# Performance work log

Measured on AMD Instinct MI355X. Metric: run time of the kernel, lower is better.

## Reference

```python
import jax, jax.numpy as jnp
import numpy as np

N, D, M, H, FF, L = 8192, 14, 36, 256, 2048, 2  # rows, d_model, material feats, mlp hidden, ffn, layers
EPS = 1e-5


def _ln(x, g, b):
    mu = jnp.mean(x, axis=-1, keepdims=True)
    var = jnp.mean((x - mu) ** 2, axis=-1, keepdims=True)
    return (x - mu) * jax.lax.rsqrt(var + EPS) * g + b


def setup_inputs() -> dict:
    key = jax.random.key(0)
    ks = iter(jax.random.split(key, 32))
    p = lambda shape, fan: jax.random.normal(next(ks), shape, jnp.float32) * (fan ** -0.5)
    return {
        "x": jax.random.normal(next(ks), (N, D), jnp.float32),
        "y": jax.random.normal(next(ks), (N, M), jnp.float32),
        # 2 post-LN TransformerEncoderLayers (nhead=1, dim_feedforward=2048, relu)
        "attn_wqkv": p((L, 3 * D, D), D), "attn_bqkv": p((L, 3 * D), D),
        "attn_wo": p((L, D, D), D), "attn_bo": p((L, D), D),
        "ln1_g": jnp.ones((L, D)), "ln1_b": jnp.zeros((L, D)),
        "ff_w1": p((L, FF, D), D), "ff_b1": p((L, FF), D),
        "ff_w2": p((L, D, FF), FF), "ff_b2": p((L, D), FF),
        "ln2_g": jnp.ones((L, D)), "ln2_b": jnp.zeros((L, D)),
        "fc1_w": p((D, D), D), "fc1_b": p((D,), D),
        "fc2_w": p((1, D), D), "fc2_b": p((1,), D),
        "fc3_w": p((H, D + M + 1), D + M + 1), "fc3_b": p((H,), D + M + 1),
        "fc4_w": p((H, H), H), "fc4_b": p((H,), H),
        "fc5_w": p((1, H), H), "fc5_b": p((1,), H),
    }


def reference(x, y, attn_wqkv, attn_bqkv, attn_wo, attn_bo, ln1_g, ln1_b,
              ff_w1, ff_b1, ff_w2, ff_b2, ln2_g, ln2_b,
              fc1_w, fc1_b, fc2_w, fc2_b, fc3_w, fc3_b, fc4_w, fc4_b, fc5_w, fc5_b):
    h = x  # [N, D]; batch of size 1 squeezed away
    for l in range(L):
        qkv = h @ attn_wqkv[l].T + attn_bqkv[l]            # [N, 3D]
        q, k, v = jnp.split(qkv, 3, axis=-1)
        scores = (q @ k.T) * (D ** -0.5)                   # [N, N]
        a = jax.nn.softmax(scores, axis=-1) @ v            # [N, D]
        a = a @ attn_wo[l].T + attn_bo[l]
        h = _ln(h + a, ln1_g[l], ln1_b[l])
        f = jax.nn.relu(h @ ff_w1[l].T + ff_b1[l]) @ ff_w2[l].T + ff_b2[l]
        h = _ln(h + f, ln2_g[l], ln2_b[l])
    x1 = h @ fc1_w.T + fc1_b                               # [N, D]
    size_out = (x1 @ fc2_w.T + fc2_b)[:, 0]                # [N]

    # batched replacement of the per-row python loop
    size_int = size_out.astype(jnp.int32)                  # trunc toward zero, like .int()
    size_f = size_int.astype(jnp.float32)[:, None]         # [N, 1]
    reg_in = jnp.concatenate([size_f, x, y], axis=1)       # [N, 1+D+M]
    r = jax.nn.relu(reg_in @ fc3_w.T + fc3_b)
    r = jax.nn.relu(r @ fc4_w.T + fc4_b)
    reg_values = (r @ fc5_w.T + fc5_b)[:, 0]               # [N]
    reg_values = jnp.where(size_int != 0, reg_values, 0.0)
    return size_out, reg_values
```

## Files before the change

kernel.cpp:

```cpp
#include <hip/hip_runtime.h>
#include <math.h>

#define NN 8192
#define DD 14
#define DP 16
#define FF 2048
#define HID 256
#define LN_EPS 1e-5f
#define QSCALE (1.4426950408889634f / 3.7416573867739413f)

typedef short bf16x8 __attribute__((ext_vector_type(8)));
typedef float f32x4 __attribute__((ext_vector_type(4)));

#define LOAD16(dst, srcp) { \
  const float4* _p = (const float4*)(srcp); \
  float4 _a = _p[0], _b = _p[1], _c = _p[2], _d = _p[3]; \
  dst[0]=_a.x; dst[1]=_a.y; dst[2]=_a.z; dst[3]=_a.w; \
  dst[4]=_b.x; dst[5]=_b.y; dst[6]=_b.z; dst[7]=_b.w; \
  dst[8]=_c.x; dst[9]=_c.y; dst[10]=_c.z; dst[11]=_c.w; \
  dst[12]=_d.x; dst[13]=_d.y; dst[14]=_d.z; dst[15]=_d.w; }

#define STORE16(dstp, src) { \
  float4* _p = (float4*)(dstp); \
  _p[0] = make_float4(src[0], src[1], src[2], src[3]); \
  _p[1] = make_float4(src[4], src[5], src[6], src[7]); \
  _p[2] = make_float4(src[8], src[9], src[10], src[11]); \
  _p[3] = make_float4(src[12], src[13], src[14], src[15]); }

static __device__ __forceinline__ float fast_exp2(float x) {
#if __has_builtin(__builtin_amdgcn_exp2f)
  return __builtin_amdgcn_exp2f(x);
#else
  return exp2f(x);
#endif
}

static __device__ __forceinline__ unsigned short bf_hi(float x) {
  return (unsigned short)(__float_as_uint(x) >> 16);
}
static __device__ __forceinline__ float bf_hi_f(float x) {
  return __uint_as_float(__float_as_uint(x) & 0xffff0000u);
}

static __device__ __forceinline__ void split8(const float* pv, bf16x8* ph, bf16x8* pl) {
  #pragma unroll
  for (int i = 0; i < 8; i++) {
    unsigned int u = __float_as_uint(pv[i]);
    (*ph)[i] = (short)(u >> 16);
    float rr = pv[i] - __uint_as_float(u & 0xffff0000u);
    (*pl)[i] = (short)(__float_as_uint(rr) >> 16);
  }
}

static __device__ __forceinline__ void qkv_compute_store(
    int r, const float* hr, const float* __restrict__ wqkv,
    const float* __restrict__ bqkv, unsigned int* __restrict__ Qpack,
    unsigned int* __restrict__ KB1, unsigned int* __restrict__ KB2,
    unsigned short* __restrict__ VhiT, unsigned short* __restrict__ VloT) {
  float q[14], k[14], v[14];
  #pragma unroll 6
  for (int c = 0; c < 42; c++) {
    const float* w = wqkv + c * 14;
    float s = bqkv[c];
    #pragma unroll
    for (int d = 0; d < 14; d++) s = fmaf(hr[d], w[d], s);
    if (c < 14)       q[c] = s * QSCALE;
    else if (c < 28)  k[c - 14] = s;
    else              v[c - 28] = s;
  }
  unsigned int qp[16], k1[16], k2[16];
  unsigned short qh[14], ql[14], kh[14], kl[14];
  #pragma unroll
  for (int d = 0; d < 14; d++) {
    qh[d] = bf_hi(q[d]);
    ql[d] = bf_hi(q[d] - bf_hi_f(q[d]));
    kh[d] = bf_hi(k[d]);
    kl[d] = bf_hi(k[d] - bf_hi_f(k[d]));
  }
  #pragma unroll
  for (int i = 0; i < 7; i++) {
    qp[i]     = (unsigned int)qh[2*i] | ((unsigned int)qh[2*i+1] << 16);
    qp[8 + i] = (unsigned int)ql[2*i] | ((unsigned int)ql[2*i+1] << 16);
    k1[i]     = (unsigned int)kh[2*i] | ((unsigned int)kh[2*i+1] << 16);
    k1[8 + i] = k1[i];
    k2[i]     = (unsigned int)kl[2*i] | ((unsigned int)kl[2*i+1] << 16);
    k2[8 + i] = k2[i];
  }
  qp[7] = 0; qp[15] = 0; k1[7] = 0; k1[15] = 0; k2[7] = 0; k2[15] = 0;
  uint4* Qp4 = (uint4*)(Qpack + (size_t)r * 16);
  uint4* K14 = (uint4*)(KB1 + (size_t)r * 16);
  uint4* K24 = (uint4*)(KB2 + (size_t)r * 16);
  #pragma unroll
  for (int i = 0; i < 4; i++) {
    Qp4[i] = make_uint4(qp[4*i], qp[4*i+1], qp[4*i+2], qp[4*i+3]);
    K14[i] = make_uint4(k1[4*i], k1[4*i+1], k1[4*i+2], k1[4*i+3]);
    K24[i] = make_uint4(k2[4*i], k2[4*i+1], k2[4*i+2], k2[4*i+3]);
  }
  #pragma unroll
  for (int d = 0; d < 14; d++) {
    VhiT[(size_t)d * NN + r] = bf_hi(v[d]);
    VloT[(size_t)d * NN + r] = bf_hi(v[d] - bf_hi_f(v[d]));
  }
  VhiT[(size_t)14 * NN + r] = 0x3F80;
  VhiT[(size_t)15 * NN + r] = 0;
  VloT[(size_t)14 * NN + r] = 0;
  VloT[(size_t)15 * NN + r] = 0;
}

static __device__ __forceinline__ void store_apack(unsigned int* dst, const float* o) {
  unsigned int qp[16];
  unsigned short hh[14], ll[14];
  #pragma unroll
  for (int d = 0; d < 14; d++) {
    hh[d] = bf_hi(o[d]);
    ll[d] = bf_hi(o[d] - bf_hi_f(o[d]));
  }
  #pragma unroll
  for (int i = 0; i < 7; i++) {
    qp[i]     = (unsigned int)hh[2*i] | ((unsigned int)hh[2*i+1] << 16);
    qp[8 + i] = (unsigned int)ll[2*i] | ((unsigned int)ll[2*i+1] << 16);
  }
  qp[7] = 0; qp[15] = 0;
  uint4* d4 = (uint4*)dst;
  #pragma unroll
  for (int i = 0; i < 4; i++)
    d4[i] = make_uint4(qp[4*i], qp[4*i+1], qp[4*i+2], qp[4*i+3]);
}

static __device__ __forceinline__ void combine_ln1(
    const float* srow, const float* hr, const float* __restrict__ wo,
    const float* __restrict__ bo, const float* __restrict__ g,
    const float* __restrict__ b, float* o) {
  float L = srow[14];
  float inv = 1.f / L;
  float a[14];
  #pragma unroll
  for (int d = 0; d < 14; d++) a[d] = srow[d] * inv;
  float xx[14];
  #pragma unroll
  for (int i = 0; i < 14; i++) {
    float s = bo[i];
    #pragma unroll
    for (int d = 0; d < 14; d++) s = fmaf(wo[i * 14 + d], a[d], s);
    xx[i] = hr[i] + s;
  }
  float mu = 0.f;
  #pragma unroll
  for (int i = 0; i < 14; i++) mu += xx[i];
  mu *= (1.f / 14.f);
  float var = 0.f;
  #pragma unroll
  for (int i = 0; i < 14; i++) { float tt = xx[i] - mu; var = fmaf(tt, tt, var); }
  var *= (1.f / 14.f);
  float rs = rsqrtf(var + LN_EPS);
  #pragma unroll
  for (int i = 0; i < 14; i++) o[i] = fmaf((xx[i] - mu) * rs, g[i], b[i]);
  o[14] = 0.f; o[15] = 0.f;
}

__global__ void pack_all(const float* __restrict__ w3, const float* __restrict__ w4,
                         const float* __restrict__ ffw1, const float* __restrict__ ffw2,
                         const float* __restrict__ x, const float* __restrict__ wqkv,
                         const float* __restrict__ bqkv, float* __restrict__ h,
                         unsigned int* __restrict__ Qpack,
                         unsigned int* __restrict__ KB1, unsigned int* __restrict__ KB2,
                         unsigned short* __restrict__ VhiT, unsigned short* __restrict__ VloT,
                         unsigned short* __restrict__ B3h, unsigned short* __restrict__ B3l,
                         unsigned short* __restrict__ B4h, unsigned short* __restrict__ B4l,
                         unsigned int* __restrict__ W1B1, unsigned int* __restrict__ W1B2,
                         unsigned short* __restrict__ W2h, unsigned short* __restrict__ W2l) {
  const int blk = blockIdx.x, tid = threadIdx.x;
  if (blk < 32) {
    int t = blk * 256 + tid;
    int lane = t & 63, ks = (t >> 6) & 7, nt = t >> 9;
    int n = nt * 16 + (lane & 15);
    int k0 = ks * 32 + (lane >> 4) * 8;
    unsigned int h4[4], l4[4];
    #pragma unroll
    for (int jj = 0; jj < 4; jj++) {
      unsigned short h2[2], l2[2];
      #pragma unroll
      for (int e = 0; e < 2; e++) {
        float v = w4[(size_t)n * 256 + k0 + jj * 2 + e];
        h2[e] = bf_hi(v);
        l2[e] = bf_hi(v - bf_hi_f(v));
      }
      h4[jj] = (unsigned int)h2[0] | ((unsigned int)h2[1] << 16);
      l4[jj] = (unsigned int)l2[0] | ((unsigned int)l2[1] << 16);
    }
    ((uint4*)B4h)[t] = make_uint4(h4[0], h4[1], h4[2], h4[3]);
    ((uint4*)B4l)[t] = make_uint4(l4[0], l4[1], l4[2], l4[3]);
    if (ks < 2) {
      int fi = (nt * 2 + ks) * 64 + lane;
      #pragma unroll
      for (int jj = 0; jj < 4; jj++) {
        unsigned short h2[2], l2[2];
        #pragma unroll
        for (int e = 0; e < 2; e++) {
          int k = k0 + jj * 2 + e;
          float v = (k < 51) ? w3[(size_t)n * 51 + k] : 0.f;
          h2[e] = bf_hi(v);
          l2[e] = bf_hi(v - bf_hi_f(v));
        }
        h4[jj] = (unsigned int)h2[0] | ((unsigned int)h2[1] << 16);
        l4[jj] = (unsigned int)l2[0] | ((unsigned int)l2[1] << 16);
      }
      ((uint4*)B3h)[fi] = make_uint4(h4[0], h4[1], h4[2], h4[3]);
      ((uint4*)B3l)[fi] = make_uint4(l4[0], l4[1], l4[2], l4[3]);
    }
  } else if (blk < 48) {
    int t = (blk - 32) * 256 + tid;
    int l = t >> 11, j = t & 2047;
    const float* wrow = ffw1 + ((size_t)l * FF + j) * 14;
    unsigned int k1[16], k2[16];
    unsigned short kh[14], kl[14];
    #pragma unroll
    for (int d = 0; d < 14; d++) {
      float v = wrow[d];
      kh[d] = bf_hi(v);
      kl[d] = bf_hi(v - bf_hi_f(v));
    }
    #pragma unroll
    for (int i = 0; i < 7; i++) {
      k1[i] = (unsigned int)kh[2*i] | ((unsigned int)kh[2*i+1] << 16);
      k1[8 + i] = k1[i];
      k2[i] = (unsigned int)kl[2*i] | ((unsigned int)kl[2*i+1] << 16);
      k2[8 + i] = k2[i];
    }
    k1[7] = 0; k1[15] = 0; k2[7] = 0; k2[15] = 0;
    uint4* d1 = (uint4*)(W1B1 + (size_t)t * 16);
    uint4* d2 = (uint4*)(W1B2 + (size_t)t * 16);
    #pragma unroll
    for (int i = 0; i < 4; i++) {
      d1[i] = make_uint4(k1[4*i], k1[4*i+1], k1[4*i+2], k1[4*i+3]);
      d2[i] = make_uint4(k2[4*i], k2[4*i+1], k2[4*i+2], k2[4*i+3]);
    }
  } else if (blk < 64) {
    int t = (blk - 48) * 256 + tid;
    int l = t >> 11, j = t & 2047;
    #pragma unroll
    for (int d = 0; d < 16; d++) {
      float v = (d < 14) ? ffw2[((size_t)l * 14 + d) * FF + j] : 0.f;
      W2h[((size_t)l * 16 + d) * FF + j] = bf_hi(v);
      W2l[((size_t)l * 16 + d) * FF + j] = bf_hi(v - bf_hi_f(v));
    }
  } else {
    int r = (blk - 64) * 256 + tid;
    float hr[16];
    #pragma unroll
    for (int d = 0; d < 14; d++) hr[d] = x[(size_t)r * 14 + d];
    hr[14] = 0.f; hr[15] = 0.f;
    STORE16(h + (size_t)r * DP, hr);
    qkv_compute_store(r, hr, wqkv, bqkv, Qpack, KB1, KB2, VhiT, VloT);
  }
}

static __device__ __forceinline__ void attn_core(
    const bf16x8* __restrict__ Qp, const bf16x8* __restrict__ B1,
    const bf16x8* __restrict__ B2, const bf16x8* __restrict__ Vh,
    const bf16x8* __restrict__ Vl, int qbase, int wave, int lo4, int hi4,
    float (*Pl)[36], f32x4* o0, f32x4* o1) {
  const f32x4 zero = {0.f, 0.f, 0.f, 0.f};
  bf16x8 aQ0 = Qp[(size_t)(qbase + lo4) * 4 + hi4];
  bf16x8 aQ1 = Qp[(size_t)(qbase + 16 + lo4) * 4 + hi4];
  f32x4 acc0 = zero, acc1 = zero;
  const int kstart = wave * 1024;
  float4 ra0, ra1, rc0, rc1;
  const float4* p0 = (const float4*)&Pl[lo4][hi4 * 8];
  const float4* p1 = (const float4*)&Pl[16 + lo4][hi4 * 8];

  for (int c = 0; c < 32; c++) {
    const int kb = kstart + c * 32;
    if (c > 0) {
      ra0 = p0[0]; ra1 = p0[1]; rc0 = p1[0]; rc1 = p1[1];
      __asm__ volatile("" ::: "memory");
    }
    bf16x8 b1g0 = B1[(size_t)(kb + lo4) * 4 + hi4];
    bf16x8 b2g0 = B2[(size_t)(kb + lo4) * 4 + hi4];
    bf16x8 b1g1 = B1[(size_t)(kb + 16 + lo4) * 4 + hi4];
    bf16x8 b2g1 = B2[(size_t)(kb + 16 + lo4) * 4 + hi4];
    bf16x8 vh = Vh[(size_t)lo4 * 1024 + (kb >> 3) + hi4];
    bf16x8 vl = Vl[(size_t)lo4 * 1024 + (kb >> 3) + hi4];

    f32x4 s00 = __builtin_amdgcn_mfma_f32_16x16x32_bf16(aQ0, b1g0, zero, 0, 0, 0);
    f32x4 s01 = __builtin_amdgcn_mfma_f32_16x16x32_bf16(aQ0, b1g1, zero, 0, 0, 0);
    f32x4 s10 = __builtin_amdgcn_mfma_f32_16x16x32_bf16(aQ1, b1g0, zero, 0, 0, 0);
    f32x4 s11 = __builtin_amdgcn_mfma_f32_16x16x32_bf16(aQ1, b1g1, zero, 0, 0, 0);
    s00 = __builtin_amdgcn_mfma_f32_16x16x32_bf16(aQ0, b2g0, s00, 0, 0, 0);
    s01 = __builtin_amdgcn_mfma_f32_16x16x32_bf16(aQ0, b2g1, s01, 0, 0, 0);
    s10 = __builtin_amdgcn_mfma_f32_16x16x32_bf16(aQ1, b2g0, s10, 0, 0, 0);
    s11 = __builtin_amdgcn_mfma_f32_16x16x32_bf16(aQ1, b2g1, s11, 0, 0, 0);
    #pragma unroll
    for (int reg = 0; reg < 4; reg++) {
      Pl[hi4 * 4 + reg][lo4]           = fast_exp2(s00[reg]);
      Pl[hi4 * 4 + reg][16 + lo4]      = fast_exp2(s01[reg]);
      Pl[16 + hi4 * 4 + reg][lo4]      = fast_exp2(s10[reg]);
      Pl[16 + hi4 * 4 + reg][16 + lo4] = fast_exp2(s11[reg]);
    }
    if (c > 0) {
      const int kbp = kb - 32;
      bf16x8 vhp = Vh[(size_t)lo4 * 1024 + (kbp >> 3) + hi4];
      bf16x8 vlp = Vl[(size_t)lo4 * 1024 + (kbp >> 3) + hi4];
      float pv0[8] = {ra0.x, ra0.y, ra0.z, ra0.w, ra1.x, ra1.y, ra1.z, ra1.w};
      float pv1[8] = {rc0.x, rc0.y, rc0.z, rc0.w, rc1.x, rc1.y, rc1.z, rc1.w};
      bf16x8 ph0, pl0, ph1, pl1;
      split8(pv0, &ph0, &pl0);
      split8(pv1, &ph1, &pl1);
      acc0 = __builtin_amdgcn_mfma_f32_16x16x32_bf16(ph0, vhp, acc0, 0, 0, 0);
      acc1 = __builtin_amdgcn_mfma_f32_16x16x32_bf16(ph1, vhp, acc1, 0, 0, 0);
      acc0 = __builtin_amdgcn_mfma_f32_16x16x32_bf16(pl0, vhp, acc0, 0, 0, 0);
      acc1 = __builtin_amdgcn_mfma_f32_16x16x32_bf16(pl1, vhp, acc1, 0, 0, 0);
      acc0 = __builtin_amdgcn_mfma_f32_16x16x32_bf16(ph0, vlp, acc0, 0, 0, 0);
      acc1 = __builtin_amdgcn_mfma_f32_16x16x32_bf16(ph1, vlp, acc1, 0, 0, 0);
    }
  }
  {
    const int kbp = kstart + 31 * 32;
    bf16x8 vhp = Vh[(size_t)lo4 * 1024 + (kbp >> 3) + hi4];
    bf16x8 vlp = Vl[(size_t)lo4 * 1024 + (kbp >> 3) + hi4];
    float4 a0 = p0[0], a1 = p0[1], c0 = p1[0], c1 = p1[1];
    float pv0[8] = {a0.x, a0.y, a0.z, a0.w, a1.x, a1.y, a1.z, a1.w};
    float pv1[8] = {c0.x, c0.y, c0.z, c0.w, c1.x, c1.y, c1.z, c1.w};
    bf16x8 ph0, pl0, ph1, pl1;
    split8(pv0, &ph0, &pl0);
    split8(pv1, &ph1, &pl1);
    acc0 = __builtin_amdgcn_mfma_f32_16x16x32_bf16(ph0, vhp, acc0, 0, 0, 0);
    acc1 = __builtin_amdgcn_mfma_f32_16x16x32_bf16(ph1, vhp, acc1, 0, 0, 0);
    acc0 = __builtin_amdgcn_mfma_f32_16x16x32_bf16(pl0, vhp, acc0, 0, 0, 0);
    acc1 = __builtin_amdgcn_mfma_f32_16x16x32_bf16(pl1, vhp, acc1, 0, 0, 0);
    acc0 = __builtin_amdgcn_mfma_f32_16x16x32_bf16(ph0, vlp, acc0, 0, 0, 0);
    acc1 = __builtin_amdgcn_mfma_f32_16x16x32_bf16(ph1, vlp, acc1, 0, 0, 0);
  }
  *o0 = acc0; *o1 = acc1;
}

static __device__ __forceinline__ void ffn_core(
    bf16x8 aH0, bf16x8 aH1, const bf16x8* __restrict__ B1,
    const bf16x8* __restrict__ B2, const bf16x8* __restrict__ Vh,
    const bf16x8* __restrict__ Vl, const float* __restrict__ b1,
    int jstart, int lo4, int hi4, float (*Pl)[36], f32x4* o0, f32x4* o1) {
  const f32x4 zero = {0.f, 0.f, 0.f, 0.f};
  f32x4 acc0 = zero, acc1 = zero;
  float4 ra0, ra1, rc0, rc1;
  const float4* p0 = (const float4*)&Pl[lo4][hi4 * 8];
  const float4* p1 = (const float4*)&Pl[16 + lo4][hi4 * 8];

  for (int c = 0; c < 8; c++) {
    const int jb = jstart + c * 32;
    if (c > 0) {
      ra0 = p0[0]; ra1 = p0[1]; rc0 = p1[0]; rc1 = p1[1];
      __asm__ volatile("" ::: "memory");
    }
    bf16x8 b1g0 = B1[(size_t)(jb + lo4) * 4 + hi4];
    bf16x8 b2g0 = B2[(size_t)(jb + lo4) * 4 + hi4];
    bf16x8 b1g1 = B1[(size_t)(jb + 16 + lo4) * 4 + hi4];
    bf16x8 b2g1 = B2[(size_t)(jb + 16 + lo4) * 4 + hi4];
    float bb0 = b1[jb + lo4];
    float bb1 = b1[jb + 16 + lo4];

    f32x4 s00 = __builtin_amdgcn_mfma_f32_16x16x32_bf16(aH0, b1g0, zero, 0, 0, 0);
    f32x4 s01 = __builtin_amdgcn_mfma_f32_16x16x32_bf16(aH0, b1g1, zero, 0, 0, 0);
    f32x4 s10 = __builtin_amdgcn_mfma_f32_16x16x32_bf16(aH1, b1g0, zero, 0, 0, 0);
    f32x4 s11 = __builtin_amdgcn_mfma_f32_16x16x32_bf16(aH1, b1g1, zero, 0, 0, 0);
    s00 = __builtin_amdgcn_mfma_f32_16x16x32_bf16(aH0, b2g0, s00, 0, 0, 0);
    s01 = __builtin_amdgcn_mfma_f32_16x16x32_bf16(aH0, b2g1, s01, 0, 0, 0);
    s10 = __builtin_amdgcn_mfma_f32_16x16x32_bf16(aH1, b2g0, s10, 0, 0, 0);
    s11 = __builtin_amdgcn_mfma_f32_16x16x32_bf16(aH1, b2g1, s11, 0, 0, 0);
    #pragma unroll
    for (int reg = 0; reg < 4; reg++) {
      Pl[hi4 * 4 + reg][lo4]           = fmaxf(s00[reg] + bb0, 0.f);
      Pl[hi4 * 4 + reg][16 + lo4]      = fmaxf(s01[reg] + bb1, 0.f);
      Pl[16 + hi4 * 4 + reg][lo4]      = fmaxf(s10[reg] + bb0, 0.f);
      Pl[16 + hi4 * 4 + reg][16 + lo4] = fmaxf(s11[reg] + bb1, 0.f);
    }
    if (c > 0) {
      const int jbp = jb - 32;
      bf16x8 vhp = Vh[(size_t)lo4 * 256 + (jbp >> 3) + hi4];
      bf16x8 vlp = Vl[(size_t)lo4 * 256 + (jbp >> 3) + hi4];
      float pv0[8] = {ra0.x, ra0.y, ra0.z, ra0.w, ra1.x, ra1.y, ra1.z, ra1.w};
      float pv1[8] = {rc0.x, rc0.y, rc0.z, rc0.w, rc1.x, rc1.y, rc1.z, rc1.w};
      bf16x8 th0, tl0, th1, tl1;
      split8(pv0, &th0, &tl0);
      split8(pv1, &th1, &tl1);
      acc0 = __builtin_amdgcn_mfma_f32_16x16x32_bf16(th0, vhp, acc0, 0, 0, 0);
      acc1 = __builtin_amdgcn_mfma_f32_16x16x32_bf16(th1, vhp, acc1, 0, 0, 0);
      acc0 = __builtin_amdgcn_mfma_f32_16x16x32_bf16(tl0, vhp, acc0, 0, 0, 0);
      acc1 = __builtin_amdgcn_mfma_f32_16x16x32_bf16(tl1, vhp, acc1, 0, 0, 0);
      acc0 = __builtin_amdgcn_mfma_f32_16x16x32_bf16(th0, vlp, acc0, 0, 0, 0);
      acc1 = __builtin_amdgcn_mfma_f32_16x16x32_bf16(th1, vlp, acc1, 0, 0, 0);
    }
  }
  {
    const int jbp = jstart + 7 * 32;
    bf16x8 vhp = Vh[(size_t)lo4 * 256 + (jbp >> 3) + hi4];
    bf16x8 vlp = Vl[(size_t)lo4 * 256 + (jbp >> 3) + hi4];
    float4 a0 = p0[0], a1 = p0[1], c0 = p1[0], c1 = p1[1];
    float pv0[8] = {a0.x, a0.y, a0.z, a0.w, a1.x, a1.y, a1.z, a1.w};
    float pv1[8] = {c0.x, c0.y, c0.z, c0.w, c1.x, c1.y, c1.z, c1.w};
    bf16x8 th0, tl0, th1, tl1;
    split8(pv0, &th0, &tl0);
    split8(pv1, &th1, &tl1);
    acc0 = __builtin_amdgcn_mfma_f32_16x16x32_bf16(th0, vhp, acc0, 0, 0, 0);
    acc1 = __builtin_amdgcn_mfma_f32_16x16x32_bf16(th1, vhp, acc1, 0, 0, 0);
    acc0 = __builtin_amdgcn_mfma_f32_16x16x32_bf16(tl0, vhp, acc0, 0, 0, 0);
    acc1 = __builtin_amdgcn_mfma_f32_16x16x32_bf16(tl1, vhp, acc1, 0, 0, 0);
    acc0 = __builtin_amdgcn_mfma_f32_16x16x32_bf16(th0, vlp, acc0, 0, 0, 0);
    acc1 = __builtin_amdgcn_mfma_f32_16x16x32_bf16(th1, vlp, acc1, 0, 0, 0);
  }
  *o0 = acc0; *o1 = acc1;
}

#define SMEM_BYTES 57472

__global__ __launch_bounds__(512, 4) void layer0_fused(
    const unsigned int* __restrict__ Qpack, const unsigned int* __restrict__ KB1,
    const unsigned int* __restrict__ KB2, const unsigned short* __restrict__ VhiT,
    const unsigned short* __restrict__ VloT, float* __restrict__ h,
    const float* __restrict__ wo, const float* __restrict__ bo,
    const float* __restrict__ g1, const float* __restrict__ b1n,
    const unsigned int* __restrict__ W1B1, const unsigned int* __restrict__ W1B2,
    const unsigned short* __restrict__ W2h, const unsigned short* __restrict__ W2l,
    const float* __restrict__ fb1, const float* __restrict__ fb2,
    const float* __restrict__ g2, const float* __restrict__ b2n,
    const float* __restrict__ wqkv1, const float* __restrict__ bqkv1,
    unsigned int* __restrict__ Qpack1, unsigned int* __restrict__ KB1_1,
    unsigned int* __restrict__ KB2_1, unsigned short* __restrict__ VhiT1,
    unsigned short* __restrict__ VloT1) {
  __shared__ alignas(16) char smem[SMEM_BYTES];
  const int tid = threadIdx.x;
  const int wave = tid >> 6;
  const int lane = tid & 63;
  const int lo4 = lane & 15;
  const int hi4 = lane >> 4;
  const int qbase = blockIdx.x * 32;

  float (*Pl)[36] = (float(*)[36])(smem + wave * 4608);
  float (*sacc)[32][16] = (float(*)[32][16])(smem + 36864);
  float (*hrow)[16] = (float(*)[16])(smem + 53248);
  unsigned int (*Hl)[16] = (unsigned int(*)[16])(smem + 55296);

  f32x4 a0, a1;
  attn_core((const bf16x8*)Qpack, (const bf16x8*)KB1, (const bf16x8*)KB2,
            (const bf16x8*)VhiT, (const bf16x8*)VloT, qbase, wave, lo4, hi4,
            Pl, &a0, &a1);
  #pragma unroll
  for (int reg = 0; reg < 4; reg++) {
    sacc[wave][hi4 * 4 + reg][lo4] = a0[reg];
    sacc[wave][16 + hi4 * 4 + reg][lo4] = a1[reg];
  }
  __syncthreads();
  {
    int qq = tid >> 4, col = tid & 15;
    float v = 0.f;
    #pragma unroll
    for (int w = 0; w < 8; w++) v += sacc[w][qq][col];
    sacc[0][qq][col] = v;
  }
  __syncthreads();
  if (tid < 32) {
    int r = qbase + tid;
    float hr[16];
    LOAD16(hr, h + (size_t)r * DP);
    float o[16];
    combine_ln1(&sacc[0][tid][0], hr, wo, bo, g1, b1n, o);
    #pragma unroll
    for (int i = 0; i < 16; i++) hrow[tid][i] = o[i];
    store_apack(&Hl[tid][0], o);
  }
  __syncthreads();

  bf16x8 aH0 = *(const bf16x8*)&Hl[lo4][hi4 * 4];
  bf16x8 aH1 = *(const bf16x8*)&Hl[16 + lo4][hi4 * 4];
  f32x4 f0, f1;
  ffn_core(aH0, aH1, (const bf16x8*)W1B1, (const bf16x8*)W1B2,
           (const bf16x8*)W2h, (const bf16x8*)W2l, fb1, wave * 256,
           lo4, hi4, Pl, &f0, &f1);
  __syncthreads();
  #pragma unroll
  for (int reg = 0; reg < 4; reg++) {
    sacc[wave][hi4 * 4 + reg][lo4] = f0[reg];
    sacc[wave][16 + hi4 * 4 + reg][lo4] = f1[reg];
  }
  __syncthreads();
  {
    int qq = tid >> 4, col = tid & 15;
    float v = 0.f;
    #pragma unroll
    for (int w = 0; w < 8; w++) v += sacc[w][qq][col];
    sacc[0][qq][col] = v;
  }
  __syncthreads();
  if (tid < 32) {
    int r = qbase + tid;
    float xx[14];
    #pragma unroll
    for (int i = 0; i < 14; i++) xx[i] = hrow[tid][i] + sacc[0][tid][i] + fb2[i];
    float mu = 0.f;
    #pragma unroll
    for (int i = 0; i < 14; i++) mu += xx[i];
    mu *= (1.f / 14.f);
    float var = 0.f;
    #pragma unroll
    for (int i = 0; i < 14; i++) { float tt = xx[i] - mu; var = fmaf(tt, tt, var); }
    var *= (1.f / 14.f);
    float rs = rsqrtf(var + LN_EPS);
    float o[16];
    #pragma unroll
    for (int i = 0; i < 14; i++) o[i] = fmaf((xx[i] - mu) * rs, g2[i], b2n[i]);
    o[14] = 0.f; o[15] = 0.f;
    STORE16(h + (size_t)r * DP, o);
    qkv_compute_store(r, o, wqkv1, bqkv1, Qpack1, KB1_1, KB2_1, VhiT1, VloT1);
  }
}

__global__ __launch_bounds__(512, 4) void layer1_tail(
    const unsigned int* __restrict__ Qpack, const unsigned int* __restrict__ KB1,
    const unsigned int* __restrict__ KB2, const unsigned short* __restrict__ VhiT,
    const unsigned short* __restrict__ VloT, const float* __restrict__ h,
    const float* __restrict__ wo, const float* __restrict__ bo,
    const float* __restrict__ g1, const float* __restrict__ b1n,
    const unsigned int* __restrict__ W1B1, const unsigned int* __restrict__ W1B2,
    const unsigned short* __restrict__ W2h, const unsigned short* __restrict__ W2l,
    const float* __restrict__ fb1, const float* __restrict__ fb2,
    const float* __restrict__ g2, const float* __restrict__ b2n,
    const float* __restrict__ fc1w, const float* __restrict__ fc1b,
    const float* __restrict__ fc2w, const float* __restrict__ fc2b,
    const float* __restrict__ x, const float* __restrict__ y,
    const unsigned short* __restrict__ B3h, const unsigned short* __restrict__ B3l,
    const float* __restrict__ b3,
    const unsigned short* __restrict__ B4h, const unsigned short* __restrict__ B4l,
    const float* __restrict__ b4,
    const float* __restrict__ w5, const float* __restrict__ b5,
    float* __restrict__ out, float* __restrict__ outr) {
  __shared__ alignas(16) char smem[SMEM_BYTES];
  const int tid = threadIdx.x;
  const int wave = tid >> 6;
  const int lane = tid & 63;
  const int lo4 = lane & 15;
  const int hi4 = lane >> 4;
  const int qbase = blockIdx.x * 32;
  const f32x4 zero = {0.f, 0.f, 0.f, 0.f};

  float (*Pl)[36] = (float(*)[36])(smem + wave * 4608);
  float (*sacc)[32][16] = (float(*)[32][16])(smem + 36864);
  float (*hrow)[16] = (float(*)[16])(smem + 53248);
  unsigned int (*Hl)[16] = (unsigned int(*)[16])(smem + 55296);
  float* szf = (float*)(smem + 57344);

  f32x4 a0, a1;
  attn_core((const bf16x8*)Qpack, (const bf16x8*)KB1, (const bf16x8*)KB2,
            (const bf16x8*)VhiT, (const bf16x8*)VloT, qbase, wave, lo4, hi4,
            Pl, &a0, &a1);
  #pragma unroll
  for (int reg = 0; reg < 4; reg++) {
    sacc[wave][hi4 * 4 + reg][lo4] = a0[reg];
    sacc[wave][16 + hi4 * 4 + reg][lo4] = a1[reg];
  }
  __syncthreads();
  {
    int qq = tid >> 4, col = tid & 15;
    float v = 0.f;
    #pragma unroll
    for (int w = 0; w < 8; w++) v += sacc[w][qq][col];
    sacc[0][qq][col] = v;
  }
  __syncthreads();
  if (tid < 32) {
    int r = qbase + tid;
    float hr[16];
    LOAD16(hr, h + (size_t)r * DP);
    float o[16];
    combine_ln1(&sacc[0][tid][0], hr, wo, bo, g1, b1n, o);
    #pragma unroll
    for (int i = 0; i < 16; i++) hrow[tid][i] = o[i];
    store_apack(&Hl[tid][0], o);
  }
  __syncthreads();

  bf16x8 aH0 = *(const bf16x8*)&Hl[lo4][hi4 * 4];
  bf16x8 aH1 = *(const bf16x8*)&Hl[16 + lo4][hi4 * 4];
  f32x4 f0, f1;
  ffn_core(aH0, aH1, (const bf16x8*)W1B1, (const bf16x8*)W1B2,
           (const bf16x8*)W2h, (const bf16x8*)W2l, fb1, wave * 256,
           lo4, hi4, Pl, &f0, &f1);
  __syncthreads();
  #pragma unroll
  for (int reg = 0; reg < 4; reg++) {
    sacc[wave][hi4 * 4 + reg][lo4] = f0[reg];
    sacc[wave][16 + hi4 * 4 + reg][lo4] = f1[reg];
  }
  __syncthreads();
  {
    int qq = tid >> 4, col = tid & 15;
    float v = 0.f;
    #pragma unroll
    for (int w = 0; w < 8; w++) v += sacc[w][qq][col];
    sacc[0][qq][col] = v;
  }
  __syncthreads();
  if (tid < 32) {
    int r = qbase + tid;
    float xx[14];
    #pragma unroll
    for (int i = 0; i < 14; i++) xx[i] = hrow[tid][i] + sacc[0][tid][i] + fb2[i];
    float mu = 0.f;
    #pragma unroll
    for (int i = 0; i < 14; i++) mu += xx[i];
    mu *= (1.f / 14.f);
    float var = 0.f;
    #pragma unroll
    for (int i = 0; i < 14; i++) { float tt = xx[i] - mu; var = fmaf(tt, tt, var); }
    var *= (1.f / 14.f);
    float rs = rsqrtf(var + LN_EPS);
    float o[14];
    #pragma unroll
    for (int i = 0; i < 14; i++) o[i] = fmaf((xx[i] - mu) * rs, g2[i], b2n[i]);
    float s = fc2b[0];
    #pragma unroll
    for (int i = 0; i < 14; i++) {
      float tt = fc1b[i];
      #pragma unroll
      for (int d = 0; d < 14; d++) tt = fmaf(fc1w[i * 14 + d], o[d], tt);
      s = fmaf(tt, fc2w[i], s);
    }
    out[r] = s;
    int si = (int)s;
    szf[tid] = (float)si;
  }
  __syncthreads();

  const int grp = wave >> 2;
  const int wg  = wave & 3;

  for (int idx = tid; idx < 2 * 16 * 64; idx += 512) {
    int g = idx >> 10, m = (idx >> 6) & 15, k = idx & 63;
    int r = qbase + g * 16 + m;
    float v = 0.f;
    if (k == 0)       v = szf[g * 16 + m];
    else if (k < 15)  v = x[(size_t)r * 14 + (k - 1)];
    else if (k < 51)  v = y[(size_t)r * 36 + (k - 15)];
    ((unsigned short(*)[72])(smem + g * 2304))[m][k] = bf_hi(v);
    ((unsigned short(*)[72])(smem + 4608 + g * 2304))[m][k] = bf_hi(v - bf_hi_f(v));
  }
  __syncthreads();

  unsigned short (*Ah)[72]  = (unsigned short(*)[72])(smem + grp * 2304);
  unsigned short (*Al)[72]  = (unsigned short(*)[72])(smem + 4608 + grp * 2304);
  unsigned short (*R1h)[264] = (unsigned short(*)[264])(smem + 9216 + grp * 8448);
  unsigned short (*R1l)[264] = (unsigned short(*)[264])(smem + 26112 + grp * 8448);
  float (*sred)[16][16] = (float(*)[16][16])(smem + 43008 + (size_t)grp * 4096);

  f32x4 acc[4];
  #pragma unroll
  for (int nt = 0; nt < 4; nt++) acc[nt] = zero;
  #pragma unroll
  for (int ks = 0; ks < 2; ks++) {
    bf16x8 ah = *(const bf16x8*)&Ah[lo4][ks * 32 + hi4 * 8];
    bf16x8 al = *(const bf16x8*)&Al[lo4][ks * 32 + hi4 * 8];
    #pragma unroll
    for (int nt = 0; nt < 4; nt++) {
      int fi = ((wg * 4 + nt) * 2 + ks) * 64 + lane;
      bf16x8 bh = ((const bf16x8*)B3h)[fi];
      bf16x8 bl = ((const bf16x8*)B3l)[fi];
      acc[nt] = __builtin_amdgcn_mfma_f32_16x16x32_bf16(ah, bh, acc[nt], 0, 0, 0);
      acc[nt] = __builtin_amdgcn_mfma_f32_16x16x32_bf16(al, bh, acc[nt], 0, 0, 0);
      acc[nt] = __builtin_amdgcn_mfma_f32_16x16x32_bf16(ah, bl, acc[nt], 0, 0, 0);
    }
  }
  #pragma unroll
  for (int nt = 0; nt < 4; nt++) {
    int n = (wg * 4 + nt) * 16 + lo4;
    float bbv = b3[n];
    #pragma unroll
    for (int reg = 0; reg < 4; reg++) {
      int m = hi4 * 4 + reg;
      float v = fmaxf(acc[nt][reg] + bbv, 0.f);
      R1h[m][n] = bf_hi(v);
      R1l[m][n] = bf_hi(v - bf_hi_f(v));
    }
  }
  __syncthreads();

  #pragma unroll
  for (int nt = 0; nt < 4; nt++) acc[nt] = zero;
  #pragma unroll
  for (int ks = 0; ks < 8; ks++) {
    bf16x8 ah = *(const bf16x8*)&R1h[lo4][ks * 32 + hi4 * 8];
    bf16x8 al = *(const bf16x8*)&R1l[lo4][ks * 32 + hi4 * 8];
    #pragma unroll
    for (int nt = 0; nt < 4; nt++) {
      int fi = ((wg * 4 + nt) * 8 + ks) * 64 + lane;
      bf16x8 bh = ((const bf16x8*)B4h)[fi];
      bf16x8 bl = ((const bf16x8*)B4l)[fi];
      acc[nt] = __builtin_amdgcn_mfma_f32_16x16x32_bf16(ah, bh, acc[nt], 0, 0, 0);
      acc[nt] = __builtin_amdgcn_mfma_f32_16x16x32_bf16(al, bh, acc[nt], 0, 0, 0);
      acc[nt] = __builtin_amdgcn_mfma_f32_16x16x32_bf16(ah, bl, acc[nt], 0, 0, 0);
    }
  }
  float s4[4] = {0.f, 0.f, 0.f, 0.f};
  #pragma unroll
  for (int nt = 0; nt < 4; nt++) {
    int n = (wg * 4 + nt) * 16 + lo4;
    float bbv = b4[n], ww = w5[n];
    #pragma unroll
    for (int reg = 0; reg < 4; reg++)
      s4[reg] = fmaf(fmaxf(acc[nt][reg] + bbv, 0.f), ww, s4[reg]);
  }
  #pragma unroll
  for (int reg = 0; reg < 4; reg++) sred[wg][hi4 * 4 + reg][lo4] = s4[reg];
  __syncthreads();

  if (tid < 32) {
    int g = tid >> 4, m = tid & 15;
    float (*sredG)[16][16] = (float(*)[16][16])(smem + 43008 + (size_t)g * 4096);
    float t = b5[0];
    #pragma unroll
    for (int w = 0; w < 4; w++) {
      const float4* p = (const float4*)&sredG[w][m][0];
      float4 q0 = p[0], q1 = p[1], q2 = p[2], q3 = p[3];
      t += ((q0.x + q0.y) + (q0.z + q0.w)) + ((q1.x + q1.y) + (q1.z + q1.w)) +
           ((q2.x + q2.y) + (q2.z + q2.w)) + ((q3.x + q3.y) + (q3.z + q3.w));
    }
    float sz = szf[tid];
    outr[qbase + tid] = (sz != 0.f) ? t : 0.f;
  }
}

extern "C" void kernel_launch(void* const* d_in, const int* in_sizes, int n_in,
                              void* d_out, int out_size, void* d_ws, size_t ws_size,
                              hipStream_t stream) {
  const float* x    = (const float*)d_in[0];
  const float* y    = (const float*)d_in[1];
  const float* wqkv = (const float*)d_in[2];
  const float* bqkv = (const float*)d_in[3];
  const float* wo   = (const float*)d_in[4];
  const float* bo   = (const float*)d_in[5];
  const float* ln1g = (const float*)d_in[6];
  const float* ln1b = (const float*)d_in[7];
  const float* ffw1 = (const float*)d_in[8];
  const float* ffb1 = (const float*)d_in[9];
  const float* ffw2 = (const float*)d_in[10];
  const float* ffb2 = (const float*)d_in[11];
  const float* ln2g = (const float*)d_in[12];
  const float* ln2b = (const float*)d_in[13];
  const float* fc1w = (const float*)d_in[14];
  const float* fc1b = (const float*)d_in[15];
  const float* fc2w = (const float*)d_in[16];
  const float* fc2b = (const float*)d_in[17];
  const float* fc3w = (const float*)d_in[18];
  const float* fc3b = (const float*)d_in[19];
  const float* fc4w = (const float*)d_in[20];
  const float* fc4b = (const float*)d_in[21];
  const float* fc5w = (const float*)d_in[22];
  const float* fc5b = (const float*)d_in[23];

  float* ws = (float*)d_ws;
  float*          h      = ws;
  unsigned int*   Qpack0 = (unsigned int*)(ws + 131072);
  unsigned int*   KB1_0  = (unsigned int*)(ws + 262144);
  unsigned int*   KB2_0  = (unsigned int*)(ws + 393216);
  unsigned short* VhiT0  = (unsigned short*)(ws + 524288);
  unsigned short* VloT0  = (unsigned short*)(ws + 589824);
  unsigned int*   Qpack1 = (unsigned int*)(ws + 786432);
  unsigned int*   KB1_1  = (unsigned int*)(ws + 917504);
  unsigned int*   KB2_1  = (unsigned int*)(ws + 1048576);
  unsigned short* VhiT1  = (unsigned short*)(ws + 1179648);
  unsigned short* VloT1  = (unsigned short*)(ws + 1245184);
  unsigned short* B3h    = (unsigned short*)(ws + 2891776);
  unsigned short* B3l    = (unsigned short*)(ws + 2899968);
  unsigned short* B4h    = (unsigned short*)(ws + 2908160);
  unsigned short* B4l    = (unsigned short*)(ws + 2940928);
  unsigned int*   W1B1   = (unsigned int*)(ws + 2973696);
  unsigned int*   W1B2   = (unsigned int*)(ws + 3039232);
  unsigned short* W2h    = (unsigned short*)(ws + 3104768);
  unsigned short* W2l    = (unsigned short*)(ws + 3137536);

  float* out = (float*)d_out;

  pack_all<<<96, 256, 0, stream>>>(fc3w, fc4w, ffw1, ffw2, x, wqkv, bqkv, h,
                                   Qpack0, KB1_0, KB2_0, VhiT0, VloT0,
                                   B3h, B3l, B4h, B4l, W1B1, W1B2, W2h, W2l);

  layer0_fused<<<256, 512, 0, stream>>>(
      Qpack0, KB1_0, KB2_0, VhiT0, VloT0, h,
      wo, bo, ln1g, ln1b,
      W1B1, W1B2, W2h, W2l, ffb1, ffb2, ln2g, ln2b,
      wqkv + 42 * 14, bqkv + 42,
      Qpack1, KB1_1, KB2_1, VhiT1, VloT1);

  layer1_tail<<<256, 512, 0, stream>>>(
      Qpack1, KB1_1, KB2_1, VhiT1, VloT1, h,
      wo + 196, bo + 14, ln1g + 14, ln1b + 14,
      W1B1 + (size_t)2048 * 16, W1B2 + (size_t)2048 * 16,
      W2h + (size_t)16 * FF, W2l + (size_t)16 * FF,
      ffb1 + FF, ffb2 + 14, ln2g + 14, ln2b + 14,
      fc1w, fc1b, fc2w, fc2b, x, y,
      B3h, B3l, fc3b, B4h, B4l, fc4b,
      fc5w, fc5b, out, out + NN);
}
```

Measured before the change: 231.1 us.

## Split attention and FFN key ranges across 16 waves per block

```diff
diff --git a/kernel.cpp b/kernel.cpp
--- a/kernel.cpp
+++ b/kernel.cpp
@@ -255,21 +255,21 @@
   }
 }
 
+template<int NCHUNK>
 static __device__ __forceinline__ void attn_core(
     const bf16x8* __restrict__ Qp, const bf16x8* __restrict__ B1,
     const bf16x8* __restrict__ B2, const bf16x8* __restrict__ Vh,
-    const bf16x8* __restrict__ Vl, int qbase, int wave, int lo4, int hi4,
+    const bf16x8* __restrict__ Vl, int qbase, int kstart, int lo4, int hi4,
     float (*Pl)[36], f32x4* o0, f32x4* o1) {
   const f32x4 zero = {0.f, 0.f, 0.f, 0.f};
   bf16x8 aQ0 = Qp[(size_t)(qbase + lo4) * 4 + hi4];
   bf16x8 aQ1 = Qp[(size_t)(qbase + 16 + lo4) * 4 + hi4];
   f32x4 acc0 = zero, acc1 = zero;
-  const int kstart = wave * 1024;
   float4 ra0, ra1, rc0, rc1;
   const float4* p0 = (const float4*)&Pl[lo4][hi4 * 8];
   const float4* p1 = (const float4*)&Pl[16 + lo4][hi4 * 8];
 
-  for (int c = 0; c < 32; c++) {
+  for (int c = 0; c < NCHUNK; c++) {
     const int kb = kstart + c * 32;
     if (c > 0) {
       ra0 = p0[0]; ra1 = p0[1]; rc0 = p1[0]; rc1 = p1[1];
@@ -315,7 +315,7 @@
     }
   }
   {
-    const int kbp = kstart + 31 * 32;
+    const int kbp = kstart + (NCHUNK - 1) * 32;
     bf16x8 vhp = Vh[(size_t)lo4 * 1024 + (kbp >> 3) + hi4];
     bf16x8 vlp = Vl[(size_t)lo4 * 1024 + (kbp >> 3) + hi4];
     float4 a0 = p0[0], a1 = p0[1], c0 = p1[0], c1 = p1[1];
@@ -334,6 +334,7 @@
   *o0 = acc0; *o1 = acc1;
 }
 
+template<int NCHUNK>
 static __device__ __forceinline__ void ffn_core(
     bf16x8 aH0, bf16x8 aH1, const bf16x8* __restrict__ B1,
     const bf16x8* __restrict__ B2, const bf16x8* __restrict__ Vh,
@@ -345,7 +346,7 @@
   const float4* p0 = (const float4*)&Pl[lo4][hi4 * 8];
   const float4* p1 = (const float4*)&Pl[16 + lo4][hi4 * 8];
 
-  for (int c = 0; c < 8; c++) {
+  for (int c = 0; c < NCHUNK; c++) {
     const int jb = jstart + c * 32;
     if (c > 0) {
       ra0 = p0[0]; ra1 = p0[1]; rc0 = p1[0]; rc1 = p1[1];
@@ -391,7 +392,7 @@
     }
   }
   {
-    const int jbp = jstart + 7 * 32;
+    const int jbp = jstart + (NCHUNK - 1) * 32;
     bf16x8 vhp = Vh[(size_t)lo4 * 256 + (jbp >> 3) + hi4];
     bf16x8 vlp = Vl[(size_t)lo4 * 256 + (jbp >> 3) + hi4];
     float4 a0 = p0[0], a1 = p0[1], c0 = p1[0], c1 = p1[1];
@@ -410,9 +411,9 @@
   *o0 = acc0; *o1 = acc1;
 }
 
-#define SMEM_BYTES 57472
-
-__global__ __launch_bounds__(512, 4) void layer0_fused(
+#define SMEM_BYTES 77952
+
+__global__ __launch_bounds__(1024, 1) void layer0_fused(
     const unsigned int* __restrict__ Qpack, const unsigned int* __restrict__ KB1,
     const unsigned int* __restrict__ KB2, const unsigned short* __restrict__ VhiT,
     const unsigned short* __restrict__ VloT, float* __restrict__ h,
@@ -435,25 +436,26 @@
   const int qbase = blockIdx.x * 32;
 
   float (*Pl)[36] = (float(*)[36])(smem + wave * 4608);
-  float (*sacc)[32][16] = (float(*)[32][16])(smem + 36864);
-  float (*hrow)[16] = (float(*)[16])(smem + 53248);
-  unsigned int (*Hl)[16] = (unsigned int(*)[16])(smem + 55296);
+  float (*sacc)[32][16] = (float(*)[32][16])(smem);
+  float (*hrow)[16] = (float(*)[16])(smem + 73728);
+  unsigned int (*Hl)[16] = (unsigned int(*)[16])(smem + 75776);
 
   f32x4 a0, a1;
-  attn_core((const bf16x8*)Qpack, (const bf16x8*)KB1, (const bf16x8*)KB2,
-            (const bf16x8*)VhiT, (const bf16x8*)VloT, qbase, wave, lo4, hi4,
-            Pl, &a0, &a1);
+  attn_core<16>((const bf16x8*)Qpack, (const bf16x8*)KB1, (const bf16x8*)KB2,
+                (const bf16x8*)VhiT, (const bf16x8*)VloT, qbase, wave * 512,
+                lo4, hi4, Pl, &a0, &a1);
+  __syncthreads();
   #pragma unroll
   for (int reg = 0; reg < 4; reg++) {
     sacc[wave][hi4 * 4 + reg][lo4] = a0[reg];
     sacc[wave][16 + hi4 * 4 + reg][lo4] = a1[reg];
   }
   __syncthreads();
-  {
+  if (tid < 512) {
     int qq = tid >> 4, col = tid & 15;
     float v = 0.f;
     #pragma unroll
-    for (int w = 0; w < 8; w++) v += sacc[w][qq][col];
+    for (int w = 0; w < 16; w++) v += sacc[w][qq][col];
     sacc[0][qq][col] = v;
   }
   __syncthreads();
@@ -472,9 +474,9 @@
   bf16x8 aH0 = *(const bf16x8*)&Hl[lo4][hi4 * 4];
   bf16x8 aH1 = *(const bf16x8*)&Hl[16 + lo4][hi4 * 4];
   f32x4 f0, f1;
-  ffn_core(aH0, aH1, (const bf16x8*)W1B1, (const bf16x8*)W1B2,
-           (const bf16x8*)W2h, (const bf16x8*)W2l, fb1, wave * 256,
-           lo4, hi4, Pl, &f0, &f1);
+  ffn_core<4>(aH0, aH1, (const bf16x8*)W1B1, (const bf16x8*)W1B2,
+              (const bf16x8*)W2h, (const bf16x8*)W2l, fb1, wave * 128,
+              lo4, hi4, Pl, &f0, &f1);
   __syncthreads();
   #pragma unroll
   for (int reg = 0; reg < 4; reg++) {
@@ -482,11 +484,11 @@
     sacc[wave][16 + hi4 * 4 + reg][lo4] = f1[reg];
   }
   __syncthreads();
-  {
+  if (tid < 512) {
     int qq = tid >> 4, col = tid & 15;
     float v = 0.f;
     #pragma unroll
-    for (int w = 0; w < 8; w++) v += sacc[w][qq][col];
+    for (int w = 0; w < 16; w++) v += sacc[w][qq][col];
     sacc[0][qq][col] = v;
   }
   __syncthreads();
@@ -513,7 +515,7 @@
   }
 }
 
-__global__ __launch_bounds__(512, 4) void layer1_tail(
+__global__ __launch_bounds__(1024, 1) void layer1_tail(
     const unsigned int* __restrict__ Qpack, const unsigned int* __restrict__ KB1,
     const unsigned int* __restrict__ KB2, const unsigned short* __restrict__ VhiT,
     const unsigned short* __restrict__ VloT, const float* __restrict__ h,
@@ -542,26 +544,27 @@
   const f32x4 zero = {0.f, 0.f, 0.f, 0.f};
 
   float (*Pl)[36] = (float(*)[36])(smem + wave * 4608);
-  float (*sacc)[32][16] = (float(*)[32][16])(smem + 36864);
-  float (*hrow)[16] = (float(*)[16])(smem + 53248);
-  unsigned int (*Hl)[16] = (unsigned int(*)[16])(smem + 55296);
-  float* szf = (float*)(smem + 57344);
+  float (*sacc)[32][16] = (float(*)[32][16])(smem);
+  float (*hrow)[16] = (float(*)[16])(smem + 73728);
+  unsigned int (*Hl)[16] = (unsigned int(*)[16])(smem + 75776);
+  float* szf = (float*)(smem + 77824);
 
   f32x4 a0, a1;
-  attn_core((const bf16x8*)Qpack, (const bf16x8*)KB1, (const bf16x8*)KB2,
-            (const bf16x8*)VhiT, (const bf16x8*)VloT, qbase, wave, lo4, hi4,
-            Pl, &a0, &a1);
+  attn_core<16>((const bf16x8*)Qpack, (const bf16x8*)KB1, (const bf16x8*)KB2,
+                (const bf16x8*)VhiT, (const bf16x8*)VloT, qbase, wave * 512,
+                lo4, hi4, Pl, &a0, &a1);
+  __syncthreads();
   #pragma unroll
   for (int reg = 0; reg < 4; reg++) {
     sacc[wave][hi4 * 4 + reg][lo4] = a0[reg];
     sacc[wave][16 + hi4 * 4 + reg][lo4] = a1[reg];
   }
   __syncthreads();
-  {
+  if (tid < 512) {
     int qq = tid >> 4, col = tid & 15;
     float v = 0.f;
     #pragma unroll
-    for (int w = 0; w < 8; w++) v += sacc[w][qq][col];
+    for (int w = 0; w < 16; w++) v += sacc[w][qq][col];
     sacc[0][qq][col] = v;
   }
   __syncthreads();
@@ -580,9 +583,9 @@
   bf16x8 aH0 = *(const bf16x8*)&Hl[lo4][hi4 * 4];
   bf16x8 aH1 = *(const bf16x8*)&Hl[16 + lo4][hi4 * 4];
   f32x4 f0, f1;
-  ffn_core(aH0, aH1, (const bf16x8*)W1B1, (const bf16x8*)W1B2,
-           (const bf16x8*)W2h, (const bf16x8*)W2l, fb1, wave * 256,
-           lo4, hi4, Pl, &f0, &f1);
+  ffn_core<4>(aH0, aH1, (const bf16x8*)W1B1, (const bf16x8*)W1B2,
+              (const bf16x8*)W2h, (const bf16x8*)W2l, fb1, wave * 128,
+              lo4, hi4, Pl, &f0, &f1);
   __syncthreads();
   #pragma unroll
   for (int reg = 0; reg < 4; reg++) {
@@ -590,11 +593,11 @@
     sacc[wave][16 + hi4 * 4 + reg][lo4] = f1[reg];
   }
   __syncthreads();
-  {
+  if (tid < 512) {
     int qq = tid >> 4, col = tid & 15;
     float v = 0.f;
     #pragma unroll
-    for (int w = 0; w < 8; w++) v += sacc[w][qq][col];
+    for (int w = 0; w < 16; w++) v += sacc[w][qq][col];
     sacc[0][qq][col] = v;
   }
   __syncthreads();
@@ -629,10 +632,10 @@
   }
   __syncthreads();
 
-  const int grp = wave >> 2;
-  const int wg  = wave & 3;
-
-  for (int idx = tid; idx < 2 * 16 * 64; idx += 512) {
+  const int grp = wave >> 3;
+  const int wg  = wave & 7;
+
+  for (int idx = tid; idx < 2 * 16 * 64; idx += 1024) {
     int g = idx >> 10, m = (idx >> 6) & 15, k = idx & 63;
     int r = qbase + g * 16 + m;
     float v = 0.f;
@@ -648,18 +651,18 @@
   unsigned short (*Al)[72]  = (unsigned short(*)[72])(smem + 4608 + grp * 2304);
   unsigned short (*R1h)[264] = (unsigned short(*)[264])(smem + 9216 + grp * 8448);
   unsigned short (*R1l)[264] = (unsigned short(*)[264])(smem + 26112 + grp * 8448);
-  float (*sred)[16][16] = (float(*)[16][16])(smem + 43008 + (size_t)grp * 4096);
-
-  f32x4 acc[4];
-  #pragma unroll
-  for (int nt = 0; nt < 4; nt++) acc[nt] = zero;
+  float (*sred)[16][16] = (float(*)[16][16])(smem + 43008 + (size_t)grp * 8192);
+
+  f32x4 acc[2];
+  #pragma unroll
+  for (int nt = 0; nt < 2; nt++) acc[nt] = zero;
   #pragma unroll
   for (int ks = 0; ks < 2; ks++) {
     bf16x8 ah = *(const bf16x8*)&Ah[lo4][ks * 32 + hi4 * 8];
     bf16x8 al = *(const bf16x8*)&Al[lo4][ks * 32 + hi4 * 8];
     #pragma unroll
-    for (int nt = 0; nt < 4; nt++) {
-      int fi = ((wg * 4 + nt) * 2 + ks) * 64 + lane;
+    for (int nt = 0; nt < 2; nt++) {
+      int fi = ((wg * 2 + nt) * 2 + ks) * 64 + lane;
       bf16x8 bh = ((const bf16x8*)B3h)[fi];
       bf16x8 bl = ((const bf16x8*)B3l)[fi];
       acc[nt] = __builtin_amdgcn_mfma_f32_16x16x32_bf16(ah, bh, acc[nt], 0, 0, 0);
@@ -668,8 +671,8 @@
     }
   }
   #pragma unroll
-  for (int nt = 0; nt < 4; nt++) {
-    int n = (wg * 4 + nt) * 16 + lo4;
+  for (int nt = 0; nt < 2; nt++) {
+    int n = (wg * 2 + nt) * 16 + lo4;
     float bbv = b3[n];
     #pragma unroll
     for (int reg = 0; reg < 4; reg++) {
@@ -682,14 +685,14 @@
   __syncthreads();
 
   #pragma unroll
-  for (int nt = 0; nt < 4; nt++) acc[nt] = zero;
+  for (int nt = 0; nt < 2; nt++) acc[nt] = zero;
   #pragma unroll
   for (int ks = 0; ks < 8; ks++) {
     bf16x8 ah = *(const bf16x8*)&R1h[lo4][ks * 32 + hi4 * 8];
     bf16x8 al = *(const bf16x8*)&R1l[lo4][ks * 32 + hi4 * 8];
     #pragma unroll
-    for (int nt = 0; nt < 4; nt++) {
-      int fi = ((wg * 4 + nt) * 8 + ks) * 64 + lane;
+    for (int nt = 0; nt < 2; nt++) {
+      int fi = ((wg * 2 + nt) * 8 + ks) * 64 + lane;
       bf16x8 bh = ((const bf16x8*)B4h)[fi];
       bf16x8 bl = ((const bf16x8*)B4l)[fi];
       acc[nt] = __builtin_amdgcn_mfma_f32_16x16x32_bf16(ah, bh, acc[nt], 0, 0, 0);
@@ -699,8 +702,8 @@
   }
   float s4[4] = {0.f, 0.f, 0.f, 0.f};
   #pragma unroll
-  for (int nt = 0; nt < 4; nt++) {
-    int n = (wg * 4 + nt) * 16 + lo4;
+  for (int nt = 0; nt < 2; nt++) {
+    int n = (wg * 2 + nt) * 16 + lo4;
     float bbv = b4[n], ww = w5[n];
     #pragma unroll
     for (int reg = 0; reg < 4; reg++)
@@ -712,10 +715,10 @@
 
   if (tid < 32) {
     int g = tid >> 4, m = tid & 15;
-    float (*sredG)[16][16] = (float(*)[16][16])(smem + 43008 + (size_t)g * 4096);
+    float (*sredG)[16][16] = (float(*)[16][16])(smem + 43008 + (size_t)g * 8192);
     float t = b5[0];
     #pragma unroll
-    for (int w = 0; w < 4; w++) {
+    for (int w = 0; w < 8; w++) {
       const float4* p = (const float4*)&sredG[w][m][0];
       float4 q0 = p[0], q1 = p[1], q2 = p[2], q3 = p[3];
       t += ((q0.x + q0.y) + (q0.z + q0.w)) + ((q1.x + q1.y) + (q1.z + q1.w)) +
@@ -781,14 +784,14 @@
                                    Qpack0, KB1_0, KB2_0, VhiT0, VloT0,
                                    B3h, B3l, B4h, B4l, W1B1, W1B2, W2h, W2l);
 
-  layer0_fused<<<256, 512, 0, stream>>>(
+  layer0_fused<<<256, 1024, 0, stream>>>(
       Qpack0, KB1_0, KB2_0, VhiT0, VloT0, h,
       wo, bo, ln1g, ln1b,
       W1B1, W1B2, W2h, W2l, ffb1, ffb2, ln2g, ln2b,
       wqkv + 42 * 14, bqkv + 42,
       Qpack1, KB1_1, KB2_1, VhiT1, VloT1);
 
-  layer1_tail<<<256, 512, 0, stream>>>(
+  layer1_tail<<<256, 1024, 0, stream>>>(
       Qpack1, KB1_1, KB2_1, VhiT1, VloT1, h,
       wo + 196, bo + 14, ln1g + 14, ln1b + 14,
       W1B1 + (size_t)2048 * 16, W1B2 + (size_t)2048 * 16,
```

Measured after the change: 232.3 us. Within noise of the previous version (+0.5%).
